# Performance work log

Hardware: AMD Instinct MI355X
Metric: run time of the kernel (lower is better)

Reference implementation:

```python
import jax, jax.numpy as jnp
import numpy as np

D_MODEL = 256
N_HEAD = 8


def quick_gelu(x):
    return x * jax.nn.sigmoid(1.702 * x)


def setup_inputs() -> dict:
    key = jax.random.key(0)
    ks = jax.random.split(key, 7)
    d = D_MODEL
    s = 0.02
    return {
        "x": jax.random.normal(ks[0], (2, 512, d), dtype=jnp.float32),
        "W_qkv": jax.random.normal(ks[1], (d, 3 * d), dtype=jnp.float32) * s,
        "b_qkv": jnp.zeros((3 * d,), dtype=jnp.float32),
        "W_fc": jax.random.normal(ks[2], (d, 4 * d), dtype=jnp.float32) * s,
        "b_fc": jnp.zeros((4 * d,), dtype=jnp.float32),
        "W_proj": jax.random.normal(ks[3], (4 * d, d), dtype=jnp.float32) * s,
        "b_proj": jnp.zeros((d,), dtype=jnp.float32),
    }


def attention_l1(x, W_qkv, b_qkv):
    bs, n_ctx, width = x.shape
    h = N_HEAD
    c = width // h
    scale = 1.0 / jnp.sqrt(jnp.asarray(c, x.dtype))
    qkv = (x @ W_qkv + b_qkv).reshape(bs, n_ctx, h, 3 * c)
    q, k, v = jnp.split(qkv, 3, axis=-1)  # each (b, t, h, c)
    qh = q.transpose(0, 2, 1, 3)  # (b, h, t, c)
    kh = k.transpose(0, 2, 1, 3)  # (b, h, s, c)
    vh = v.transpose(0, 2, 1, 3)  # (b, h, s, c)
    # L1 distance: sum_c |q - k| * scale  -> (b, h, t, s)
    dist = jnp.sum(jnp.abs(qh[:, :, :, None, :] - kh[:, :, None, :, :]), axis=-1) * scale
    weight = 1.0 / (0.001 + dist)
    idx = jnp.arange(n_ctx)
    weight = weight.at[:, :, idx, idx].set(0.0)
    wdtype = weight.dtype
    weight = jax.nn.softmax(weight.astype(jnp.float32), axis=-1).astype(wdtype)
    out = jnp.einsum('bhts,bhsc->bthc', weight, vh)
    return out.reshape(bs, n_ctx, width)


def reference(x, W_qkv, b_qkv, W_fc, b_fc, W_proj, b_proj):
    x = x + attention_l1(x, W_qkv, b_qkv)
    h = quick_gelu(x @ W_fc + b_fc)
    x = x + (h @ W_proj + b_proj)
    return x
```

## Files before the change

### kernel.cpp

```cpp
#include <hip/hip_runtime.h>
#include <hip/hip_bf16.h>
#include <hip/hip_fp16.h>

#define DM   256
#define NH   8
#define HC   32
#define SEQ  512
#define MTOT 1024

#define B_X1   0
#define B_QH   (1u<<20)
#define B_KH   0x180000u
#define B_VT   0x200000u
#define B_WFCT 0x280000u
#define B_WPJT 0x300000u

typedef __attribute__((ext_vector_type(8))) __bf16 bf16x8;
typedef __attribute__((ext_vector_type(4))) __bf16 bf16x4;
typedef __attribute__((ext_vector_type(4))) float  f32x4;

__device__ __forceinline__ float qgelu(float x) {
    return x / (1.0f + __expf(-1.702f * x));
}

#define BKP 264

__global__ __launch_bounds__(256)
void qkv_k(const float* __restrict__ x, const float* __restrict__ W,
           const float* __restrict__ bias,
           const float* __restrict__ Wfc, const float* __restrict__ Wproj,
           char* __restrict__ wsb)
{
    __shared__ float lt[64 * 65];
    __shared__ __align__(16) __bf16 lbt[16 * BKP];
    const int bid = blockIdx.x, tid = threadIdx.x;

    if (bid >= 768) {
        const int tt = bid - 768;
        const float* src; __bf16* dst; int K, N, tile;
        if (tt < 64) { src = Wfc;   dst = (__bf16*)(wsb + B_WFCT); K = 256;  N = 1024; tile = tt; }
        else         { src = Wproj; dst = (__bf16*)(wsb + B_WPJT); K = 1024; N = 256;  tile = tt - 64; }
        const int nn = N >> 6;
        const int k0 = (tile / nn) * 64, n0 = (tile % nn) * 64;
        const int rr0 = tid >> 4, c4 = tid & 15;
        #pragma unroll
        for (int i = 0; i < 4; ++i) {
            const int rr = rr0 + i * 16;
            float4 v = *(const float4*)&src[(size_t)(k0 + rr) * N + n0 + c4 * 4];
            lt[rr * 65 + c4 * 4 + 0] = v.x; lt[rr * 65 + c4 * 4 + 1] = v.y;
            lt[rr * 65 + c4 * 4 + 2] = v.z; lt[rr * 65 + c4 * 4 + 3] = v.w;
        }
        __syncthreads();
        #pragma unroll
        for (int i = 0; i < 4; ++i) {
            const int rr = rr0 + i * 16;
            bf16x4 b;
            b.x = (__bf16)lt[(c4 * 4 + 0) * 65 + rr];
            b.y = (__bf16)lt[(c4 * 4 + 1) * 65 + rr];
            b.z = (__bf16)lt[(c4 * 4 + 2) * 65 + rr];
            b.w = (__bf16)lt[(c4 * 4 + 3) * 65 + rr];
            *(bf16x4*)&dst[(size_t)(n0 + rr) * K + k0 + c4 * 4] = b;
        }
        return;
    }

    const int lane = tid & 63, wv = tid >> 6;
    const int n0 = (bid >> 4) * 16;
    const int m0 = ((bid * 4 + wv) & 63) * 16;
    const int r = lane & 15, q = lane >> 4;

    {
        const int kk = tid >> 2;
        const int c4 = (tid & 3) * 4;
        #pragma unroll
        for (int p = 0; p < 4; ++p) {
            const int k = p * 64 + kk;
            float4 w = *(const float4*)&W[(size_t)k * 768 + n0 + c4];
            lbt[(c4 + 0) * BKP + k] = (__bf16)w.x;
            lbt[(c4 + 1) * BKP + k] = (__bf16)w.y;
            lbt[(c4 + 2) * BKP + k] = (__bf16)w.z;
            lbt[(c4 + 3) * BKP + k] = (__bf16)w.w;
        }
    }
    __syncthreads();

    const float*  ap = x + (size_t)(m0 + r) * DM + q * 8;
    const __bf16* bl = &lbt[r * BKP + q * 8];

    f32x4 acc = {0.f, 0.f, 0.f, 0.f};
    #pragma unroll
    for (int kt = 0; kt < DM; kt += 32) {
        float4 a0 = *(const float4*)(ap + kt);
        float4 a1 = *(const float4*)(ap + kt + 4);
        bf16x8 af;
        af[0] = (__bf16)a0.x; af[1] = (__bf16)a0.y; af[2] = (__bf16)a0.z; af[3] = (__bf16)a0.w;
        af[4] = (__bf16)a1.x; af[5] = (__bf16)a1.y; af[6] = (__bf16)a1.z; af[7] = (__bf16)a1.w;
        bf16x8 bf = *(const bf16x8*)(bl + kt);
        acc = __builtin_amdgcn_mfma_f32_16x16x32_bf16(af, bf, acc, 0, 0, 0);
    }

    __half*  qh  = (__half*)(wsb + B_QH);
    __half*  kh  = (__half*)(wsb + B_KH);
    __bf16*  vtb = (__bf16*)(wsb + B_VT);
    const int n = n0 + r;
    const float bn = bias[n];
    const int h = n / 96, jj = n % 96;
    #pragma unroll
    for (int i = 0; i < 4; ++i) {
        const int m = m0 + q * 4 + i;
        const float v = acc[i] + bn;
        const int b = m >> 9, t = m & 511;
        const int bh = b * NH + h;
        if (jj < 32)      qh[((size_t)(bh * SEQ + t)) * HC + jj]        = (__half)v;
        else if (jj < 64) kh[((size_t)(bh * SEQ + t)) * HC + (jj - 32)] = (__half)v;
        else              vtb[((size_t)(bh * HC + (jj - 64))) * SEQ + t] = (__bf16)v;
    }
}

#define QT 16
#define PSTRIDE 514

__global__ __launch_bounds__(512, 4)
void attn_k(const char* __restrict__ wsb, const float* __restrict__ xin,
            float* __restrict__ x1, const float* __restrict__ bproj,
            float* __restrict__ out)
{
    __shared__ __half2 qtile[QT * 16];
    __shared__ __bf16  pmat[QT * PSTRIDE];
    __shared__ float   psum[QT * 8];
    __shared__ float   pinv[QT];

    const __half*  qhg = (const __half*)(wsb + B_QH);
    const __half*  khg = (const __half*)(wsb + B_KH);
    const __bf16*  vtb = (const __bf16*)(wsb + B_VT);

    const int tid  = threadIdx.x;
    const int lane = tid & 63;
    const int wv   = tid >> 6;
    const int sg   = tid;
    const int bh   = blockIdx.x >> 5;
    const int qbase = (blockIdx.x & 31) * QT;
    const float scale = 0.17677669529663687f;

    const __half2* kp = (const __half2*)(khg + ((size_t)(bh * SEQ + sg)) * HC);
    __half2 kr[16];
    #pragma unroll
    for (int j = 0; j < 16; ++j) kr[j] = kp[j];

    if (tid < 256) {
        const int t = tid >> 4, j = tid & 15;
        qtile[t * 16 + j] =
            *(const __half2*)(qhg + ((size_t)(bh * SEQ + qbase + t)) * HC + j * 2);
    }
    __syncthreads();

    #pragma unroll 4
    for (int t = 0; t < QT; ++t) {
        __half2 acc2 = __floats2half2_rn(0.f, 0.f);
        #pragma unroll
        for (int j = 0; j < 16; ++j) {
            __half2 dif = __hsub2(kr[j], qtile[t * 16 + j]);
            unsigned u = (*(unsigned*)&dif) & 0x7FFF7FFFu;
            acc2 = __hadd2(acc2, *(__half2*)&u);
        }
        const float d = __low2float(acc2) + __high2float(acc2);
        float w = 1.0f / (0.001f + d * scale);
        if (sg == qbase + t) w = 0.0f;
        float p = __expf(w);
        float se = p;
        #pragma unroll
        for (int off = 32; off >= 1; off >>= 1) se += __shfl_xor(se, off, 64);
        pmat[t * PSTRIDE + sg] = (__bf16)p;
        if (lane == 0) psum[t * 8 + wv] = se;
    }
    __syncthreads();

    if (tid < QT) {
        float s = 0.f;
        #pragma unroll
        for (int j = 0; j < 8; ++j) s += psum[tid * 8 + j];
        pinv[tid] = 1.0f / s;
    }
    __syncthreads();

    if (wv < 2) {
        const int r = lane & 15, q = lane >> 4;
        const __bf16* bp  = vtb + ((size_t)(bh * HC + wv * 16 + r)) * SEQ + q * 8;
        const __bf16* apm = &pmat[r * PSTRIDE + q * 8];
        f32x4 acc = {0.f, 0.f, 0.f, 0.f};
        #pragma unroll
        for (int kt = 0; kt < SEQ; kt += 32) {
            bf16x8 af = *(const bf16x8*)(apm + kt);
            bf16x8 bf = *(const bf16x8*)(bp + kt);
            acc = __builtin_amdgcn_mfma_f32_16x16x32_bf16(af, bf, acc, 0, 0, 0);
        }
        const int b = bh >> 3, hh = bh & 7;
        const int c = wv * 16 + r;
        const int col = hh * HC + c;
        const float bpn = bproj[col];
        #pragma unroll
        for (int i = 0; i < 4; ++i) {
            const int tl = q * 4 + i;
            const int t  = qbase + tl;
            const float v = acc[i] * pinv[tl];
            const int idx = ((b * SEQ + t) * DM) + col;
            const float res = xin[idx] + v;
            x1[idx]  = res;
            out[idx] = res + bpn;
        }
    }
}

#define HSTR 264

__global__ __launch_bounds__(512)
void mlp_k(const float* __restrict__ X1, const char* __restrict__ wsb,
           const float* __restrict__ bfc, float* __restrict__ out)
{
    __shared__ __align__(16) __bf16 hs[16 * HSTR];
    const __bf16* Wf = (const __bf16*)(wsb + B_WFCT);
    const __bf16* Wp = (const __bf16*)(wsb + B_WPJT);

    const int tid  = threadIdx.x;
    const int lane = tid & 63;
    const int wv   = tid >> 6;
    const int mt   = blockIdx.x & 63;
    const int ns   = blockIdx.x >> 6;
    const int m0   = mt * 16;
    const int r    = lane & 15, q = lane >> 4;

    bf16x8 wp[16];
    #pragma unroll
    for (int kt8 = 0; kt8 < 8; ++kt8)
        #pragma unroll
        for (int nt = 0; nt < 2; ++nt)
            wp[kt8 * 2 + nt] = *(const bf16x8*)(Wp +
                (size_t)(wv * 32 + nt * 16 + r) * 1024 + ns * 256 + kt8 * 32 + q * 8);

    {
        const float* ap = X1 + (size_t)(m0 + r) * DM + q * 8;

        bf16x8 afr[8];
        #pragma unroll
        for (int kt8 = 0; kt8 < 8; ++kt8) {
            float4 a0 = *(const float4*)(ap + kt8 * 32);
            float4 a1 = *(const float4*)(ap + kt8 * 32 + 4);
            bf16x8 af;
            af[0] = (__bf16)a0.x; af[1] = (__bf16)a0.y; af[2] = (__bf16)a0.z; af[3] = (__bf16)a0.w;
            af[4] = (__bf16)a1.x; af[5] = (__bf16)a1.y; af[6] = (__bf16)a1.z; af[7] = (__bf16)a1.w;
            afr[kt8] = af;
        }

        f32x4 acc[2] = {};
        #pragma unroll
        for (int kt8 = 0; kt8 < 8; ++kt8) {
            #pragma unroll
            for (int nt = 0; nt < 2; ++nt) {
                const int n0 = ns * 256 + (wv * 2 + nt) * 16;
                bf16x8 bf = *(const bf16x8*)(Wf + (size_t)(n0 + r) * DM + kt8 * 32 + q * 8);
                acc[nt] = __builtin_amdgcn_mfma_f32_16x16x32_bf16(afr[kt8], bf, acc[nt], 0, 0, 0);
            }
        }
        #pragma unroll
        for (int nt = 0; nt < 2; ++nt) {
            const int nl = (wv * 2 + nt) * 16 + r;
            const float bn = bfc[ns * 256 + nl];
            #pragma unroll
            for (int i = 0; i < 4; ++i)
                hs[(q * 4 + i) * HSTR + nl] = (__bf16)qgelu(acc[nt][i] + bn);
        }
    }
    __syncthreads();

    {
        f32x4 acc[2] = {};
        const __bf16* al = &hs[r * HSTR + q * 8];
        #pragma unroll
        for (int kt8 = 0; kt8 < 8; ++kt8) {
            bf16x8 af = *(const bf16x8*)(al + kt8 * 32);
            acc[0] = __builtin_amdgcn_mfma_f32_16x16x32_bf16(af, wp[kt8 * 2 + 0], acc[0], 0, 0, 0);
            acc[1] = __builtin_amdgcn_mfma_f32_16x16x32_bf16(af, wp[kt8 * 2 + 1], acc[1], 0, 0, 0);
        }
        #pragma unroll
        for (int nt = 0; nt < 2; ++nt) {
            const int n = wv * 32 + nt * 16 + r;
            #pragma unroll
            for (int i = 0; i < 4; ++i) {
                const int m = m0 + q * 4 + i;
                atomicAdd(&out[(size_t)m * DM + n], acc[nt][i]);
            }
        }
    }
}

extern "C" void kernel_launch(void* const* d_in, const int* in_sizes, int n_in,
                              void* d_out, int out_size, void* d_ws, size_t ws_size,
                              hipStream_t stream)
{
    (void)in_sizes; (void)n_in; (void)out_size; (void)ws_size;
    const float* x     = (const float*)d_in[0];
    const float* Wqkv  = (const float*)d_in[1];
    const float* bqkv  = (const float*)d_in[2];
    const float* Wfc   = (const float*)d_in[3];
    const float* bfc   = (const float*)d_in[4];
    const float* Wproj = (const float*)d_in[5];
    const float* bproj = (const float*)d_in[6];
    float* out = (float*)d_out;
    char*  wsb = (char*)d_ws;
    float* x1  = (float*)(wsb + B_X1);

    qkv_k<<<896, 256, 0, stream>>>(x, Wqkv, bqkv, Wfc, Wproj, wsb);

    attn_k<<<512, 512, 0, stream>>>(wsb, x, x1, bproj, out);

    mlp_k<<<256, 512, 0, stream>>>(x1, wsb, bfc, out);
}
```

Measured before the change: 106.3 us.

## Split PV reduction across all waves and move weight transposes into attention launch

The P·V MFMA stage in the attention kernel now runs on all eight waves: each wave covers one quarter of the key dimension, and the partial accumulators are reduced through shared memory before the epilogue. Before, only two waves did this work. The MLP weight transpose/convert blocks move from the QKV kernel into extra blocks of the attention kernel, and the shared memory is unioned so the extra tile buffer does not raise the attention kernel's LDS footprint. This shortens the QKV kernel's tail and spreads the PV work, at the cost of an extra barrier and a shared-memory reduction.

```diff
diff --git a/kernel.cpp b/kernel.cpp
--- a/kernel.cpp
+++ b/kernel.cpp
@@ -27,42 +27,10 @@
 
 __global__ __launch_bounds__(256)
 void qkv_k(const float* __restrict__ x, const float* __restrict__ W,
-           const float* __restrict__ bias,
-           const float* __restrict__ Wfc, const float* __restrict__ Wproj,
-           char* __restrict__ wsb)
+           const float* __restrict__ bias, char* __restrict__ wsb)
 {
-    __shared__ float lt[64 * 65];
     __shared__ __align__(16) __bf16 lbt[16 * BKP];
     const int bid = blockIdx.x, tid = threadIdx.x;
-
-    if (bid >= 768) {
-        const int tt = bid - 768;
-        const float* src; __bf16* dst; int K, N, tile;
-        if (tt < 64) { src = Wfc;   dst = (__bf16*)(wsb + B_WFCT); K = 256;  N = 1024; tile = tt; }
-        else         { src = Wproj; dst = (__bf16*)(wsb + B_WPJT); K = 1024; N = 256;  tile = tt - 64; }
-        const int nn = N >> 6;
-        const int k0 = (tile / nn) * 64, n0 = (tile % nn) * 64;
-        const int rr0 = tid >> 4, c4 = tid & 15;
-        #pragma unroll
-        for (int i = 0; i < 4; ++i) {
-            const int rr = rr0 + i * 16;
-            float4 v = *(const float4*)&src[(size_t)(k0 + rr) * N + n0 + c4 * 4];
-            lt[rr * 65 + c4 * 4 + 0] = v.x; lt[rr * 65 + c4 * 4 + 1] = v.y;
-            lt[rr * 65 + c4 * 4 + 2] = v.z; lt[rr * 65 + c4 * 4 + 3] = v.w;
-        }
-        __syncthreads();
-        #pragma unroll
-        for (int i = 0; i < 4; ++i) {
-            const int rr = rr0 + i * 16;
-            bf16x4 b;
-            b.x = (__bf16)lt[(c4 * 4 + 0) * 65 + rr];
-            b.y = (__bf16)lt[(c4 * 4 + 1) * 65 + rr];
-            b.z = (__bf16)lt[(c4 * 4 + 2) * 65 + rr];
-            b.w = (__bf16)lt[(c4 * 4 + 3) * 65 + rr];
-            *(bf16x4*)&dst[(size_t)(n0 + rr) * K + k0 + c4 * 4] = b;
-        }
-        return;
-    }
 
     const int lane = tid & 63, wv = tid >> 6;
     const int n0 = (bid >> 4) * 16;
@@ -119,27 +87,67 @@
 
 #define QT 16
 #define PSTRIDE 514
+#define O_QTILE  16448
+#define O_PSUM   17472
+#define O_PINV   17984
+#define O_PART   18048
+#define SMSZ     26240
 
 __global__ __launch_bounds__(512, 4)
 void attn_k(const char* __restrict__ wsb, const float* __restrict__ xin,
             float* __restrict__ x1, const float* __restrict__ bproj,
-            float* __restrict__ out)
+            const float* __restrict__ Wfc, const float* __restrict__ Wproj,
+            float* __restrict__ out, char* __restrict__ wsw)
 {
-    __shared__ __half2 qtile[QT * 16];
-    __shared__ __bf16  pmat[QT * PSTRIDE];
-    __shared__ float   psum[QT * 8];
-    __shared__ float   pinv[QT];
+    __shared__ __align__(16) unsigned char SM[SMSZ];
+    const int tid = threadIdx.x;
+    const int bid = blockIdx.x;
+
+    if (bid >= 512) {
+        const int tt = bid - 512;
+        const float* src; __bf16* dst; int K, N, tile;
+        if (tt < 64) { src = Wfc;   dst = (__bf16*)(wsw + B_WFCT); K = 256;  N = 1024; tile = tt; }
+        else         { src = Wproj; dst = (__bf16*)(wsw + B_WPJT); K = 1024; N = 256;  tile = tt - 64; }
+        float* lt = (float*)SM;
+        const int nn = N >> 6;
+        const int k0 = (tile / nn) * 64, n0 = (tile % nn) * 64;
+        const int rr0 = tid >> 4, c4 = tid & 15;
+        #pragma unroll
+        for (int i = 0; i < 2; ++i) {
+            const int rr = rr0 + i * 32;
+            float4 v = *(const float4*)&src[(size_t)(k0 + rr) * N + n0 + c4 * 4];
+            lt[rr * 65 + c4 * 4 + 0] = v.x; lt[rr * 65 + c4 * 4 + 1] = v.y;
+            lt[rr * 65 + c4 * 4 + 2] = v.z; lt[rr * 65 + c4 * 4 + 3] = v.w;
+        }
+        __syncthreads();
+        #pragma unroll
+        for (int i = 0; i < 2; ++i) {
+            const int rr = rr0 + i * 32;
+            bf16x4 b;
+            b.x = (__bf16)lt[(c4 * 4 + 0) * 65 + rr];
+            b.y = (__bf16)lt[(c4 * 4 + 1) * 65 + rr];
+            b.z = (__bf16)lt[(c4 * 4 + 2) * 65 + rr];
+            b.w = (__bf16)lt[(c4 * 4 + 3) * 65 + rr];
+            *(bf16x4*)&dst[(size_t)(n0 + rr) * K + k0 + c4 * 4] = b;
+        }
+        return;
+    }
+
+    __bf16*  pmat  = (__bf16*)SM;
+    __half2* qtile = (__half2*)(SM + O_QTILE);
+    float*   psum  = (float*)(SM + O_PSUM);
+    float*   pinv  = (float*)(SM + O_PINV);
+    float*   part  = (float*)(SM + O_PART);
 
     const __half*  qhg = (const __half*)(wsb + B_QH);
     const __half*  khg = (const __half*)(wsb + B_KH);
     const __bf16*  vtb = (const __bf16*)(wsb + B_VT);
 
-    const int tid  = threadIdx.x;
     const int lane = tid & 63;
     const int wv   = tid >> 6;
     const int sg   = tid;
-    const int bh   = blockIdx.x >> 5;
-    const int qbase = (blockIdx.x & 31) * QT;
+    const int bh   = bid >> 5;
+    const int qbase = (bid & 31) * QT;
     const float scale = 0.17677669529663687f;
 
     const __half2* kp = (const __half2*)(khg + ((size_t)(bh * SEQ + sg)) * HC);
@@ -183,31 +191,37 @@
     }
     __syncthreads();
 
-    if (wv < 2) {
+    {
         const int r = lane & 15, q = lane >> 4;
-        const __bf16* bp  = vtb + ((size_t)(bh * HC + wv * 16 + r)) * SEQ + q * 8;
-        const __bf16* apm = &pmat[r * PSTRIDE + q * 8];
+        const int nc = wv & 1, ks = wv >> 1;
+        const __bf16* bp  = vtb + ((size_t)(bh * HC + nc * 16 + r)) * SEQ + ks * 128 + q * 8;
+        const __bf16* apm = &pmat[r * PSTRIDE + ks * 128 + q * 8];
         f32x4 acc = {0.f, 0.f, 0.f, 0.f};
         #pragma unroll
-        for (int kt = 0; kt < SEQ; kt += 32) {
+        for (int kt = 0; kt < 128; kt += 32) {
             bf16x8 af = *(const bf16x8*)(apm + kt);
             bf16x8 bf = *(const bf16x8*)(bp + kt);
             acc = __builtin_amdgcn_mfma_f32_16x16x32_bf16(af, bf, acc, 0, 0, 0);
         }
+        *(f32x4*)&part[wv * 256 + lane * 4] = acc;
+    }
+    __syncthreads();
+
+    {
+        const int nc  = tid >> 8;
+        const int idx = tid & 255;
+        float s = part[(0 * 2 + nc) * 256 + idx] + part[(1 * 2 + nc) * 256 + idx]
+                + part[(2 * 2 + nc) * 256 + idx] + part[(3 * 2 + nc) * 256 + idx];
+        const int colr = (idx >> 2) & 15;
+        const int tl   = ((idx >> 6) << 2) + (idx & 3);
+        const int t    = qbase + tl;
         const int b = bh >> 3, hh = bh & 7;
-        const int c = wv * 16 + r;
-        const int col = hh * HC + c;
-        const float bpn = bproj[col];
-        #pragma unroll
-        for (int i = 0; i < 4; ++i) {
-            const int tl = q * 4 + i;
-            const int t  = qbase + tl;
-            const float v = acc[i] * pinv[tl];
-            const int idx = ((b * SEQ + t) * DM) + col;
-            const float res = xin[idx] + v;
-            x1[idx]  = res;
-            out[idx] = res + bpn;
-        }
+        const int col = hh * HC + nc * 16 + colr;
+        const float v = s * pinv[tl];
+        const int idxg = ((b * SEQ + t) * DM) + col;
+        const float res = xin[idxg] + v;
+        x1[idxg]  = res;
+        out[idxg] = res + bproj[col];
     }
 }
 
@@ -309,9 +323,9 @@
     char*  wsb = (char*)d_ws;
     float* x1  = (float*)(wsb + B_X1);
 
-    qkv_k<<<896, 256, 0, stream>>>(x, Wqkv, bqkv, Wfc, Wproj, wsb);
-
-    attn_k<<<512, 512, 0, stream>>>(wsb, x, x1, bproj, out);
+    qkv_k<<<768, 256, 0, stream>>>(x, Wqkv, bqkv, wsb);
+
+    attn_k<<<640, 512, 0, stream>>>(wsb, x, x1, bproj, Wfc, Wproj, out, wsb);
 
     mlp_k<<<256, 512, 0, stream>>>(x1, wsb, bfc, out);
 }
```

Measured after the change: 106.2 us. About the same (-0.1%).
